# Kernel tuning notes

Measured on AMD Instinct MI355X. Metric: run time of the kernel, lower is better.

## Reference

```python
import jax, jax.numpy as jnp
import numpy as np

NUM_EXPERTS = 8
TOP_K = 2
HIDDEN = 2048
INTER = 7168
NUM_TOKENS = 8192


def setup_inputs() -> dict:
    key = jax.random.key(0)
    k0, k1, k2, k3, k4 = jax.random.split(key, 5)
    hidden_states = jax.random.normal(k0, (NUM_TOKENS, HIDDEN), dtype=jnp.float32)
    gate_w = jax.random.normal(k1, (NUM_EXPERTS, HIDDEN), dtype=jnp.float32) / 10.0
    w1 = jax.random.normal(k2, (NUM_EXPERTS, INTER, HIDDEN), dtype=jnp.float32) / 10.0
    w3 = jax.random.normal(k3, (NUM_EXPERTS, INTER, HIDDEN), dtype=jnp.float32) / 10.0
    w2 = jax.random.normal(k4, (NUM_EXPERTS, HIDDEN, INTER), dtype=jnp.float32) / 10.0
    return {"hidden_states": hidden_states, "gate_w": gate_w, "w1": w1, "w3": w3, "w2": w2}


def reference(hidden_states, gate_w, w1, w3, w2):
    x = hidden_states  # [T, H]
    num_experts = gate_w.shape[0]
    # router
    router_logits = x @ gate_w.T  # [T, E]
    probs = jax.nn.softmax(router_logits.astype(jnp.float32), axis=-1)
    top_w, top_i = jax.lax.top_k(probs, TOP_K)              # [T, K]
    top_w = top_w / jnp.sum(top_w, axis=-1, keepdims=True)  # renormalize
    top_w = top_w.astype(x.dtype)
    # dense [T, E] routing weight (0 for unselected experts)
    expert_ids = jnp.arange(num_experts)
    w_dense = jnp.sum(
        jnp.where(top_i[:, :, None] == expert_ids[None, None, :], top_w[:, :, None], 0.0),
        axis=1,
    )  # [T, E]
    out = jnp.zeros_like(x)
    for e in range(num_experts):
        g = jax.nn.silu(x @ w1[e].T) * (x @ w3[e].T)  # [T, I]
        out = out + w_dense[:, e:e + 1] * (g @ w2[e].T)
    return out
```

## Files before the change

kernel.cpp:

```cpp
#include <hip/hip_runtime.h>

#define NTOK 8192
#define HID 2048
#define ITR 7168
#define NE 8
#define BK32 32
#define TILE32 (128 * BK32)

typedef __attribute__((ext_vector_type(8))) short short8;
typedef __attribute__((ext_vector_type(8))) __bf16 bf16x8;
typedef __attribute__((ext_vector_type(4))) float f32x4;

__device__ __forceinline__ unsigned short f2bf(float f) {
  unsigned int u = __float_as_uint(f);
  u += 0x7FFFu + ((u >> 16) & 1u);
  return (unsigned short)(u >> 16);
}

__device__ __forceinline__ f32x4 mfma_bf16(short8 a, short8 b, f32x4 c) {
  union U { short8 s; bf16x8 b; };
  U ua; ua.s = a;
  U ub; ub.s = b;
  return __builtin_amdgcn_mfma_f32_16x16x32_bf16(ua.b, ub.b, c, 0, 0, 0);
}

typedef __attribute__((address_space(1))) const unsigned int g_u32;
typedef __attribute__((address_space(3))) unsigned int l_u32;

__device__ __forceinline__ void gload16(const unsigned short* src, unsigned short* dst) {
  __builtin_amdgcn_global_load_lds((g_u32*)src, (l_u32*)dst, 16, 0, 0);
}

__device__ __forceinline__ short8 read_frag32(const unsigned short* base, int row, int kelem) {
  int slot = ((row << 2) + (kelem >> 3)) ^ (row & 7);
  return *reinterpret_cast<const short8*>(reinterpret_cast<const char*>(base) + slot * 16);
}

__device__ __forceinline__ void slot_src(int s, int* row, int* c) {
  int r0 = ((s >> 2) ^ (s >> 4)) & 1;
  *row = ((s >> 2) & ~1) | r0;
  *c = ((s ^ r0) & 1) | ((((s >> 1) ^ (s >> 3)) & 1) << 1);
}

#define VMCNT(N) asm volatile("s_waitcnt vmcnt(" #N ")" ::: "memory")
#define BARRIER()                         \
  do {                                    \
    __builtin_amdgcn_s_barrier();         \
    asm volatile("" ::: "memory");        \
  } while (0)

__global__ __launch_bounds__(256) void moe_router(
    const float* __restrict__ x, const float* __restrict__ gw,
    int* __restrict__ cnt, int* __restrict__ pair_token, float* __restrict__ pair_w) {
  int wave = threadIdx.x >> 6;
  int lane = threadIdx.x & 63;
  int t = blockIdx.x * 4 + wave;
  const float4* xr = reinterpret_cast<const float4*>(x + (size_t)t * HID);
  float acc[NE];
#pragma unroll
  for (int e = 0; e < NE; ++e) acc[e] = 0.f;
#pragma unroll
  for (int j = 0; j < 8; ++j) {
    int c = lane + 64 * j;
    float4 xv = xr[c];
#pragma unroll
    for (int e = 0; e < NE; ++e) {
      float4 gv = reinterpret_cast<const float4*>(gw + (size_t)e * HID)[c];
      acc[e] += xv.x * gv.x + xv.y * gv.y + xv.z * gv.z + xv.w * gv.w;
    }
  }
#pragma unroll
  for (int e = 0; e < NE; ++e) {
    float s = acc[e];
#pragma unroll
    for (int m = 32; m > 0; m >>= 1) s += __shfl_xor(s, m);
    acc[e] = s;
  }
  if (lane == 0) {
    int e0 = 0; float l0 = acc[0];
#pragma unroll
    for (int e = 1; e < NE; ++e) if (acc[e] > l0) { l0 = acc[e]; e0 = e; }
    int e1 = -1; float l1 = -3.0e38f;
#pragma unroll
    for (int e = 0; e < NE; ++e) if (e != e0 && acc[e] > l1) { l1 = acc[e]; e1 = e; }
    float z = __expf(l1 - l0);
    float w0 = 1.f / (1.f + z);
    float w1 = z / (1.f + z);
    int p0 = atomicAdd(&cnt[e0], 1);
    pair_token[e0 * NTOK + p0] = t;
    pair_w[e0 * NTOK + p0] = w0;
    int p1 = atomicAdd(&cnt[e1], 1);
    pair_token[e1 * NTOK + p1] = t;
    pair_w[e1 * NTOK + p1] = w1;
  }
}

__global__ void moe_scan(const int* __restrict__ cnt, int* __restrict__ base) {
  if (threadIdx.x == 0) {
    int s = 0;
#pragma unroll
    for (int e = 0; e < NE; ++e) { base[e] = s; s += cnt[e]; }
  }
}

__global__ __launch_bounds__(256) void moe_cvt(const float* __restrict__ src,
                                               unsigned short* __restrict__ dst) {
  size_t i = (size_t)blockIdx.x * 256 + threadIdx.x;
  const float4* p = reinterpret_cast<const float4*>(src) + i * 2;
  float4 a = p[0], b = p[1];
  union { unsigned short us[8]; short8 v; } u;
  u.us[0] = f2bf(a.x); u.us[1] = f2bf(a.y); u.us[2] = f2bf(a.z); u.us[3] = f2bf(a.w);
  u.us[4] = f2bf(b.x); u.us[5] = f2bf(b.y); u.us[6] = f2bf(b.z); u.us[7] = f2bf(b.w);
  reinterpret_cast<short8*>(dst)[i] = u.v;
}


__global__ __launch_bounds__(256, 2) void moe_gemm1_e(
    const unsigned short* __restrict__ xb, const unsigned short* __restrict__ w1b,
    const unsigned short* __restrict__ w3b, const int* __restrict__ cnt,
    const int* __restrict__ base, const int* __restrict__ pair_token,
    unsigned short* __restrict__ g) {
  int e = blockIdx.z;
  int n_e = cnt[e];
  int rowTile = blockIdx.x;
  if (rowTile * 128 >= n_e) return;
  int colTile = blockIdx.y;

  __shared__ unsigned short lds[3 * 3 * TILE32];

  int tid = threadIdx.x;
  int lane = tid & 63;
  int wv = tid >> 6;
  int wr = wv >> 1, wc = wv & 1;
  int lr = lane & 15;
  int lk = (lane >> 4) * 8;

  int slotP = e * NTOK + rowTile * 128;
  int slotG = base[e] + rowTile * 128;
  const unsigned short* w1e = w1b + (size_t)e * ITR * HID + (size_t)colTile * 128 * HID;
  const unsigned short* w3e = w3b + (size_t)e * ITR * HID + (size_t)colTile * 128 * HID;

  const unsigned short* a_s[2];
  const unsigned short* b1_s[2];
  const unsigned short* b3_s[2];
#pragma unroll
  for (int i = 0; i < 2; ++i) {
    int s = wv * 128 + i * 64 + lane;
    int row, c;
    slot_src(s, &row, &c);
    int tok = pair_token[slotP + ((rowTile * 128 + row < n_e) ? row : 0)];
    a_s[i] = xb + (size_t)tok * HID + c * 8;
    b1_s[i] = w1e + (size_t)row * HID + c * 8;
    b3_s[i] = w3e + (size_t)row * HID + c * 8;
  }

  f32x4 acc1[4][4], acc3[4][4];
#pragma unroll
  for (int m = 0; m < 4; ++m)
#pragma unroll
    for (int n = 0; n < 4; ++n) {
      acc1[m][n] = (f32x4){0.f, 0.f, 0.f, 0.f};
      acc3[m][n] = (f32x4){0.f, 0.f, 0.f, 0.f};
    }

#define STAGE1(buf, koff)                                                        \
  do {                                                                           \
    unsigned short* Lb = lds + (buf) * 3 * TILE32 + wv * 1024;                   \
    _Pragma("unroll") for (int i = 0; i < 2; ++i) {                              \
      gload16(a_s[i] + (koff), Lb + i * 512);                                    \
      gload16(b1_s[i] + (koff), Lb + TILE32 + i * 512);                          \
      gload16(b3_s[i] + (koff), Lb + 2 * TILE32 + i * 512);                      \
    }                                                                            \
  } while (0)

  const int nt = HID / BK32;
  STAGE1(0, 0);
  STAGE1(1, BK32);

  for (int t = 0; t < nt; ++t) {
    if (t + 1 < nt) VMCNT(6); else VMCNT(0);
    BARRIER();

    const unsigned short* A = lds + (t % 3) * 3 * TILE32;
    const unsigned short* B1 = A + TILE32;
    const unsigned short* B3 = A + 2 * TILE32;
    short8 av[4];
#pragma unroll
    for (int m = 0; m < 4; ++m) av[m] = read_frag32(A, wr * 64 + m * 16 + lr, lk);
#pragma unroll
    for (int n = 0; n < 4; ++n) {
      short8 b1v = read_frag32(B1, wc * 64 + n * 16 + lr, lk);
      short8 b3v = read_frag32(B3, wc * 64 + n * 16 + lr, lk);
#pragma unroll
      for (int m = 0; m < 4; ++m) {
        acc1[m][n] = mfma_bf16(av[m], b1v, acc1[m][n]);
        acc3[m][n] = mfma_bf16(av[m], b3v, acc3[m][n]);
      }
    }

    if (t + 2 < nt) STAGE1((t + 2) % 3, (t + 2) * BK32);
  }
#undef STAGE1

#pragma unroll
  for (int m = 0; m < 4; ++m) {
    int rbase = wr * 64 + m * 16 + ((lane >> 4) << 2);
#pragma unroll
    for (int r = 0; r < 4; ++r) {
      int rt = rbase + r;
      if (rowTile * 128 + rt < n_e) {
        unsigned short* grow = g + (size_t)(slotG + rt) * ITR + colTile * 128 + wc * 64;
#pragma unroll
        for (int n = 0; n < 4; ++n) {
          float h1 = acc1[m][n][r], h3 = acc3[m][n][r];
          float sl = h1 / (1.f + __expf(-h1));
          grow[n * 16 + lr] = f2bf(sl * h3);
        }
      }
    }
  }
}

__global__ __launch_bounds__(256, 3) void moe_gemm2_e(
    const unsigned short* __restrict__ g, const unsigned short* __restrict__ w2b,
    const int* __restrict__ cnt, const int* __restrict__ base,
    const int* __restrict__ pair_token, const float* __restrict__ pair_w,
    float* __restrict__ out) {
  int e = blockIdx.z;
  int n_e = cnt[e];
  int rowTile = blockIdx.x;
  if (rowTile * 128 >= n_e) return;
  int colTile = blockIdx.y;

  __shared__ unsigned short lds[3 * 2 * TILE32];

  int tid = threadIdx.x;
  int lane = tid & 63;
  int wv = tid >> 6;
  int wr = wv >> 1, wc = wv & 1;
  int lr = lane & 15;
  int lk = (lane >> 4) * 8;

  int slotP = e * NTOK + rowTile * 128;
  int slotG = base[e] + rowTile * 128;
  const unsigned short* w2e = w2b + (size_t)e * HID * ITR + (size_t)colTile * 128 * ITR;

  const unsigned short* a_s[2];
  const unsigned short* b_s[2];
#pragma unroll
  for (int i = 0; i < 2; ++i) {
    int s = wv * 128 + i * 64 + lane;
    int row, c;
    slot_src(s, &row, &c);
    int rclamp = (rowTile * 128 + row < n_e) ? row : 0;
    a_s[i] = g + (size_t)(slotG + rclamp) * ITR + c * 8;
    b_s[i] = w2e + (size_t)row * ITR + c * 8;
  }

  f32x4 acc[4][4];
#pragma unroll
  for (int m = 0; m < 4; ++m)
#pragma unroll
    for (int n = 0; n < 4; ++n) acc[m][n] = (f32x4){0.f, 0.f, 0.f, 0.f};

#define STAGE2(buf, koff)                                                        \
  do {                                                                           \
    unsigned short* Lb = lds + (buf) * 2 * TILE32 + wv * 1024;                   \
    _Pragma("unroll") for (int i = 0; i < 2; ++i) {                              \
      gload16(a_s[i] + (koff), Lb + i * 512);                                    \
      gload16(b_s[i] + (koff), Lb + TILE32 + i * 512);                           \
    }                                                                            \
  } while (0)

  const int nt = ITR / BK32;
  STAGE2(0, 0);
  STAGE2(1, BK32);

  for (int t = 0; t < nt; ++t) {
    if (t + 1 < nt) VMCNT(4); else VMCNT(0);
    BARRIER();

    const unsigned short* A = lds + (t % 3) * 2 * TILE32;
    const unsigned short* B = A + TILE32;
    short8 av[4];
#pragma unroll
    for (int m = 0; m < 4; ++m) av[m] = read_frag32(A, wr * 64 + m * 16 + lr, lk);
#pragma unroll
    for (int n = 0; n < 4; ++n) {
      short8 bv = read_frag32(B, wc * 64 + n * 16 + lr, lk);
#pragma unroll
      for (int m = 0; m < 4; ++m) acc[m][n] = mfma_bf16(av[m], bv, acc[m][n]);
    }

    if (t + 2 < nt) STAGE2((t + 2) % 3, (t + 2) * BK32);
  }
#undef STAGE2

#pragma unroll
  for (int m = 0; m < 4; ++m) {
    int rbase = wr * 64 + m * 16 + ((lane >> 4) << 2);
#pragma unroll
    for (int r = 0; r < 4; ++r) {
      int rt = rbase + r;
      if (rowTile * 128 + rt < n_e) {
        int slot = slotP + rt;
        int tok = pair_token[slot];
        float wgt = pair_w[slot];
        float* orow = out + (size_t)tok * HID + colTile * 128 + wc * 64;
#pragma unroll
        for (int n = 0; n < 4; ++n) atomicAdd(&orow[n * 16 + lr], wgt * acc[m][n][r]);
      }
    }
  }
}


extern "C" void kernel_launch(void* const* d_in, const int* in_sizes, int n_in,
                              void* d_out, int out_size, void* d_ws, size_t ws_size,
                              hipStream_t stream) {
  const float* x = (const float*)d_in[0];
  const float* gate_w = (const float*)d_in[1];
  const float* w1 = (const float*)d_in[2];
  const float* w3 = (const float*)d_in[3];
  const float* w2 = (const float*)d_in[4];
  float* out = (float*)d_out;

  char* ws = (char*)d_ws;
  const size_t WEL = (size_t)NE * ITR * HID;
  const size_t G_BYTES = (size_t)NTOK * 2 * ITR * 2;
  const size_t XB_BYTES = (size_t)NTOK * HID * 2;
  const size_t PAIR_BYTES = (size_t)NE * NTOK * 4;
  const size_t WB_BYTES = WEL * 2;

  unsigned short* g = (unsigned short*)ws;
  unsigned short* xb = (unsigned short*)(ws + G_BYTES);
  int* pair_token = (int*)(ws + G_BYTES + XB_BYTES);
  float* pair_w = (float*)(ws + G_BYTES + XB_BYTES + PAIR_BYTES);
  int* cnt = (int*)(ws + G_BYTES + XB_BYTES + 2 * PAIR_BYTES);
  int* base = cnt + NE;
  char* wbase = ws + G_BYTES + XB_BYTES + 2 * PAIR_BYTES + 256;
  unsigned short* w1b = (unsigned short*)wbase;
  unsigned short* w3b = (unsigned short*)(wbase + WB_BYTES);
  unsigned short* w2b = (unsigned short*)(wbase + 2 * WB_BYTES);

  hipMemsetAsync(cnt, 0, 2 * NE * sizeof(int), stream);
  hipMemsetAsync(d_out, 0, (size_t)NTOK * HID * sizeof(float), stream);

  moe_router<<<NTOK / 4, 256, 0, stream>>>(x, gate_w, cnt, pair_token, pair_w);
  moe_scan<<<1, 64, 0, stream>>>(cnt, base);
  moe_cvt<<<(NTOK * HID) / 2048, 256, 0, stream>>>(x, xb);

  const int WGRID = (int)(WEL / 2048);
  moe_cvt<<<WGRID, 256, 0, stream>>>(w1, w1b);
  moe_cvt<<<WGRID, 256, 0, stream>>>(w3, w3b);
  moe_cvt<<<WGRID, 256, 0, stream>>>(w2, w2b);

  moe_gemm1_e<<<dim3(NTOK / 128, ITR / 128, NE), 256, 0, stream>>>(
      xb, w1b, w3b, cnt, base, pair_token, g);
  moe_gemm2_e<<<dim3(NTOK / 128, HID / 128, NE), 256, 0, stream>>>(
      g, w2b, cnt, base, pair_token, pair_w, out);
}
```

Measured before the change: 3.379 ms.

## Enlarge MoE GEMM tiles, deepen pipeline, replace scatter atomics with combine kernel

```diff
diff --git a/kernel.cpp b/kernel.cpp
--- a/kernel.cpp
+++ b/kernel.cpp
@@ -5,7 +5,6 @@
 #define ITR 7168
 #define NE 8
 #define BK32 32
-#define TILE32 (128 * BK32)
 
 typedef __attribute__((ext_vector_type(8))) short short8;
 typedef __attribute__((ext_vector_type(8))) __bf16 bf16x8;
@@ -51,7 +50,8 @@
 
 __global__ __launch_bounds__(256) void moe_router(
     const float* __restrict__ x, const float* __restrict__ gw,
-    int* __restrict__ cnt, int* __restrict__ pair_token, float* __restrict__ pair_w) {
+    int* __restrict__ cnt, int* __restrict__ pair_token, float* __restrict__ pair_w,
+    int4* __restrict__ tok_ep) {
   int wave = threadIdx.x >> 6;
   int lane = threadIdx.x & 63;
   int t = blockIdx.x * 4 + wave;
@@ -92,6 +92,7 @@
     int p1 = atomicAdd(&cnt[e1], 1);
     pair_token[e1 * NTOK + p1] = t;
     pair_w[e1 * NTOK + p1] = w1;
+    tok_ep[t] = make_int4(e0, e1, p0, p1);
   }
 }
 
@@ -115,7 +116,9 @@
 }
 
 
-__global__ __launch_bounds__(256, 2) void moe_gemm1_e(
+#define G1_BUF 16384
+
+__global__ __launch_bounds__(512, 2) void moe_gemm1_f(
     const unsigned short* __restrict__ xb, const unsigned short* __restrict__ w1b,
     const unsigned short* __restrict__ w3b, const int* __restrict__ cnt,
     const int* __restrict__ base, const int* __restrict__ pair_token,
@@ -123,35 +126,41 @@
   int e = blockIdx.z;
   int n_e = cnt[e];
   int rowTile = blockIdx.x;
-  if (rowTile * 128 >= n_e) return;
+  if (rowTile * 256 >= n_e) return;
   int colTile = blockIdx.y;
 
-  __shared__ unsigned short lds[3 * 3 * TILE32];
+  __shared__ unsigned short lds[4 * G1_BUF];
 
   int tid = threadIdx.x;
   int lane = tid & 63;
   int wv = tid >> 6;
-  int wr = wv >> 1, wc = wv & 1;
+  int wr = wv >> 1;
+  int wc = wv & 1;
   int lr = lane & 15;
   int lk = (lane >> 4) * 8;
 
-  int slotP = e * NTOK + rowTile * 128;
-  int slotG = base[e] + rowTile * 128;
+  int slotP = e * NTOK + rowTile * 256;
+  int slotG = base[e] + rowTile * 256;
   const unsigned short* w1e = w1b + (size_t)e * ITR * HID + (size_t)colTile * 128 * HID;
   const unsigned short* w3e = w3b + (size_t)e * ITR * HID + (size_t)colTile * 128 * HID;
 
   const unsigned short* a_s[2];
-  const unsigned short* b1_s[2];
-  const unsigned short* b3_s[2];
+  const unsigned short* b1_s;
+  const unsigned short* b3_s;
 #pragma unroll
   for (int i = 0; i < 2; ++i) {
-    int s = wv * 128 + i * 64 + lane;
+    int s = i * 512 + wv * 64 + lane;
     int row, c;
     slot_src(s, &row, &c);
-    int tok = pair_token[slotP + ((rowTile * 128 + row < n_e) ? row : 0)];
+    int tok = pair_token[slotP + ((rowTile * 256 + row < n_e) ? row : 0)];
     a_s[i] = xb + (size_t)tok * HID + c * 8;
-    b1_s[i] = w1e + (size_t)row * HID + c * 8;
-    b3_s[i] = w3e + (size_t)row * HID + c * 8;
+  }
+  {
+    int s = wv * 64 + lane;
+    int row, c;
+    slot_src(s, &row, &c);
+    b1_s = w1e + (size_t)row * HID + c * 8;
+    b3_s = w3e + (size_t)row * HID + c * 8;
   }
 
   f32x4 acc1[4][4], acc3[4][4];
@@ -163,27 +172,29 @@
       acc3[m][n] = (f32x4){0.f, 0.f, 0.f, 0.f};
     }
 
-#define STAGE1(buf, koff)                                                        \
-  do {                                                                           \
-    unsigned short* Lb = lds + (buf) * 3 * TILE32 + wv * 1024;                   \
-    _Pragma("unroll") for (int i = 0; i < 2; ++i) {                              \
-      gload16(a_s[i] + (koff), Lb + i * 512);                                    \
-      gload16(b1_s[i] + (koff), Lb + TILE32 + i * 512);                          \
-      gload16(b3_s[i] + (koff), Lb + 2 * TILE32 + i * 512);                      \
-    }                                                                            \
+#define STAGE1(buf, koff)                                                  \
+  do {                                                                     \
+    unsigned short* Lb = lds + (buf) * G1_BUF;                             \
+    gload16(a_s[0] + (koff), Lb + (wv * 64) * 8);                          \
+    gload16(a_s[1] + (koff), Lb + (512 + wv * 64) * 8);                    \
+    gload16(b1_s + (koff), Lb + 8192 + (wv * 64) * 8);                     \
+    gload16(b3_s + (koff), Lb + 12288 + (wv * 64) * 8);                    \
   } while (0)
 
   const int nt = HID / BK32;
   STAGE1(0, 0);
   STAGE1(1, BK32);
+  STAGE1(2, 2 * BK32);
 
   for (int t = 0; t < nt; ++t) {
-    if (t + 1 < nt) VMCNT(6); else VMCNT(0);
+    if (t + 2 < nt) VMCNT(8);
+    else if (t + 1 < nt) VMCNT(4);
+    else VMCNT(0);
     BARRIER();
 
-    const unsigned short* A = lds + (t % 3) * 3 * TILE32;
-    const unsigned short* B1 = A + TILE32;
-    const unsigned short* B3 = A + 2 * TILE32;
+    const unsigned short* A = lds + (t & 3) * G1_BUF;
+    const unsigned short* B1 = A + 8192;
+    const unsigned short* B3 = A + 12288;
     short8 av[4];
 #pragma unroll
     for (int m = 0; m < 4; ++m) av[m] = read_frag32(A, wr * 64 + m * 16 + lr, lk);
@@ -198,7 +209,7 @@
       }
     }
 
-    if (t + 2 < nt) STAGE1((t + 2) % 3, (t + 2) * BK32);
+    if (t + 3 < nt) STAGE1((t + 3) & 3, (t + 3) * BK32);
   }
 #undef STAGE1
 
@@ -208,7 +219,7 @@
 #pragma unroll
     for (int r = 0; r < 4; ++r) {
       int rt = rbase + r;
-      if (rowTile * 128 + rt < n_e) {
+      if (rowTile * 256 + rt < n_e) {
         unsigned short* grow = g + (size_t)(slotG + rt) * ITR + colTile * 128 + wc * 64;
 #pragma unroll
         for (int n = 0; n < 4; ++n) {
@@ -221,96 +232,117 @@
   }
 }
 
-__global__ __launch_bounds__(256, 3) void moe_gemm2_e(
+#define G2_BUF 16384
+
+__global__ __launch_bounds__(512, 2) void moe_gemm2_f(
     const unsigned short* __restrict__ g, const unsigned short* __restrict__ w2b,
     const int* __restrict__ cnt, const int* __restrict__ base,
-    const int* __restrict__ pair_token, const float* __restrict__ pair_w,
-    float* __restrict__ out) {
+    const float* __restrict__ pair_w, float* __restrict__ part) {
   int e = blockIdx.z;
   int n_e = cnt[e];
   int rowTile = blockIdx.x;
-  if (rowTile * 128 >= n_e) return;
+  if (rowTile * 256 >= n_e) return;
   int colTile = blockIdx.y;
 
-  __shared__ unsigned short lds[3 * 2 * TILE32];
+  __shared__ unsigned short lds[4 * G2_BUF];
 
   int tid = threadIdx.x;
   int lane = tid & 63;
   int wv = tid >> 6;
-  int wr = wv >> 1, wc = wv & 1;
+  int wr = wv >> 2;
+  int wc = wv & 3;
   int lr = lane & 15;
   int lk = (lane >> 4) * 8;
 
-  int slotP = e * NTOK + rowTile * 128;
-  int slotG = base[e] + rowTile * 128;
-  const unsigned short* w2e = w2b + (size_t)e * HID * ITR + (size_t)colTile * 128 * ITR;
+  int slotP = e * NTOK + rowTile * 256;
+  int slotG = base[e] + rowTile * 256;
+  const unsigned short* w2e = w2b + (size_t)e * HID * ITR + (size_t)colTile * 256 * ITR;
 
   const unsigned short* a_s[2];
   const unsigned short* b_s[2];
 #pragma unroll
   for (int i = 0; i < 2; ++i) {
-    int s = wv * 128 + i * 64 + lane;
+    int s = i * 512 + wv * 64 + lane;
     int row, c;
     slot_src(s, &row, &c);
-    int rclamp = (rowTile * 128 + row < n_e) ? row : 0;
+    int rclamp = (rowTile * 256 + row < n_e) ? row : 0;
     a_s[i] = g + (size_t)(slotG + rclamp) * ITR + c * 8;
     b_s[i] = w2e + (size_t)row * ITR + c * 8;
   }
 
-  f32x4 acc[4][4];
-#pragma unroll
-  for (int m = 0; m < 4; ++m)
+  f32x4 acc[8][4];
+#pragma unroll
+  for (int m = 0; m < 8; ++m)
 #pragma unroll
     for (int n = 0; n < 4; ++n) acc[m][n] = (f32x4){0.f, 0.f, 0.f, 0.f};
 
-#define STAGE2(buf, koff)                                                        \
-  do {                                                                           \
-    unsigned short* Lb = lds + (buf) * 2 * TILE32 + wv * 1024;                   \
-    _Pragma("unroll") for (int i = 0; i < 2; ++i) {                              \
-      gload16(a_s[i] + (koff), Lb + i * 512);                                    \
-      gload16(b_s[i] + (koff), Lb + TILE32 + i * 512);                           \
-    }                                                                            \
+#define STAGE2(buf, koff)                                                  \
+  do {                                                                     \
+    unsigned short* Lb = lds + (buf) * G2_BUF;                             \
+    gload16(a_s[0] + (koff), Lb + (wv * 64) * 8);                          \
+    gload16(a_s[1] + (koff), Lb + (512 + wv * 64) * 8);                    \
+    gload16(b_s[0] + (koff), Lb + 8192 + (wv * 64) * 8);                   \
+    gload16(b_s[1] + (koff), Lb + 8192 + (512 + wv * 64) * 8);             \
   } while (0)
 
   const int nt = ITR / BK32;
   STAGE2(0, 0);
   STAGE2(1, BK32);
+  STAGE2(2, 2 * BK32);
 
   for (int t = 0; t < nt; ++t) {
-    if (t + 1 < nt) VMCNT(4); else VMCNT(0);
+    if (t + 2 < nt) VMCNT(8);
+    else if (t + 1 < nt) VMCNT(4);
+    else VMCNT(0);
     BARRIER();
 
-    const unsigned short* A = lds + (t % 3) * 2 * TILE32;
-    const unsigned short* B = A + TILE32;
-    short8 av[4];
-#pragma unroll
-    for (int m = 0; m < 4; ++m) av[m] = read_frag32(A, wr * 64 + m * 16 + lr, lk);
+    const unsigned short* A = lds + (t & 3) * G2_BUF;
+    const unsigned short* B = A + 8192;
+    short8 av[8];
+#pragma unroll
+    for (int m = 0; m < 8; ++m) av[m] = read_frag32(A, wr * 128 + m * 16 + lr, lk);
 #pragma unroll
     for (int n = 0; n < 4; ++n) {
       short8 bv = read_frag32(B, wc * 64 + n * 16 + lr, lk);
 #pragma unroll
-      for (int m = 0; m < 4; ++m) acc[m][n] = mfma_bf16(av[m], bv, acc[m][n]);
-    }
-
-    if (t + 2 < nt) STAGE2((t + 2) % 3, (t + 2) * BK32);
+      for (int m = 0; m < 8; ++m) acc[m][n] = mfma_bf16(av[m], bv, acc[m][n]);
+    }
+
+    if (t + 3 < nt) STAGE2((t + 3) & 3, (t + 3) * BK32);
   }
 #undef STAGE2
 
 #pragma unroll
-  for (int m = 0; m < 4; ++m) {
-    int rbase = wr * 64 + m * 16 + ((lane >> 4) << 2);
+  for (int m = 0; m < 8; ++m) {
+    int rbase = wr * 128 + m * 16 + ((lane >> 4) << 2);
 #pragma unroll
     for (int r = 0; r < 4; ++r) {
       int rt = rbase + r;
-      if (rowTile * 128 + rt < n_e) {
-        int slot = slotP + rt;
-        int tok = pair_token[slot];
-        float wgt = pair_w[slot];
-        float* orow = out + (size_t)tok * HID + colTile * 128 + wc * 64;
-#pragma unroll
-        for (int n = 0; n < 4; ++n) atomicAdd(&orow[n * 16 + lr], wgt * acc[m][n][r]);
+      if (rowTile * 256 + rt < n_e) {
+        float wgt = pair_w[slotP + rt];
+        float* prow = part + (size_t)(slotG + rt) * HID + colTile * 256 + wc * 64;
+#pragma unroll
+        for (int n = 0; n < 4; ++n) prow[n * 16 + lr] = wgt * acc[m][n][r];
       }
     }
+  }
+}
+
+__global__ __launch_bounds__(256) void moe_combine(
+    const float* __restrict__ part, const int4* __restrict__ tok_ep,
+    const int* __restrict__ base, float* __restrict__ out) {
+  int t = blockIdx.x;
+  int4 ep = tok_ep[t];
+  int s0 = base[ep.x] + ep.z;
+  int s1 = base[ep.y] + ep.w;
+  const float4* p0 = reinterpret_cast<const float4*>(part + (size_t)s0 * HID);
+  const float4* p1 = reinterpret_cast<const float4*>(part + (size_t)s1 * HID);
+  float4* o = reinterpret_cast<float4*>(out + (size_t)t * HID);
+#pragma unroll
+  for (int i = 0; i < 2; ++i) {
+    int idx = threadIdx.x + i * 256;
+    float4 a = p0[idx], b = p1[idx];
+    o[idx] = make_float4(a.x + b.x, a.y + b.y, a.z + b.z, a.w + b.w);
   }
 }
 
@@ -330,23 +362,25 @@
   const size_t G_BYTES = (size_t)NTOK * 2 * ITR * 2;
   const size_t XB_BYTES = (size_t)NTOK * HID * 2;
   const size_t PAIR_BYTES = (size_t)NE * NTOK * 4;
+  const size_t TOKEP_BYTES = (size_t)NTOK * 16;
   const size_t WB_BYTES = WEL * 2;
 
   unsigned short* g = (unsigned short*)ws;
   unsigned short* xb = (unsigned short*)(ws + G_BYTES);
   int* pair_token = (int*)(ws + G_BYTES + XB_BYTES);
   float* pair_w = (float*)(ws + G_BYTES + XB_BYTES + PAIR_BYTES);
-  int* cnt = (int*)(ws + G_BYTES + XB_BYTES + 2 * PAIR_BYTES);
+  int4* tok_ep = (int4*)(ws + G_BYTES + XB_BYTES + 2 * PAIR_BYTES);
+  int* cnt = (int*)(ws + G_BYTES + XB_BYTES + 2 * PAIR_BYTES + TOKEP_BYTES);
   int* base = cnt + NE;
-  char* wbase = ws + G_BYTES + XB_BYTES + 2 * PAIR_BYTES + 256;
+  char* wbase = ws + G_BYTES + XB_BYTES + 2 * PAIR_BYTES + TOKEP_BYTES + 256;
   unsigned short* w1b = (unsigned short*)wbase;
   unsigned short* w3b = (unsigned short*)(wbase + WB_BYTES);
   unsigned short* w2b = (unsigned short*)(wbase + 2 * WB_BYTES);
+  float* part = (float*)wbase;
 
   hipMemsetAsync(cnt, 0, 2 * NE * sizeof(int), stream);
-  hipMemsetAsync(d_out, 0, (size_t)NTOK * HID * sizeof(float), stream);
-
-  moe_router<<<NTOK / 4, 256, 0, stream>>>(x, gate_w, cnt, pair_token, pair_w);
+
+  moe_router<<<NTOK / 4, 256, 0, stream>>>(x, gate_w, cnt, pair_token, pair_w, tok_ep);
   moe_scan<<<1, 64, 0, stream>>>(cnt, base);
   moe_cvt<<<(NTOK * HID) / 2048, 256, 0, stream>>>(x, xb);
 
@@ -355,8 +389,9 @@
   moe_cvt<<<WGRID, 256, 0, stream>>>(w3, w3b);
   moe_cvt<<<WGRID, 256, 0, stream>>>(w2, w2b);
 
-  moe_gemm1_e<<<dim3(NTOK / 128, ITR / 128, NE), 256, 0, stream>>>(
+  moe_gemm1_f<<<dim3(NTOK / 256, ITR / 128, NE), 512, 0, stream>>>(
       xb, w1b, w3b, cnt, base, pair_token, g);
-  moe_gemm2_e<<<dim3(NTOK / 128, HID / 128, NE), 256, 0, stream>>>(
-      g, w2b, cnt, base, pair_token, pair_w, out);
-}
+  moe_gemm2_f<<<dim3(NTOK / 256, HID / 256, NE), 512, 0, stream>>>(
+      g, w2b, cnt, base, pair_w, part);
+  moe_combine<<<NTOK, 256, 0, stream>>>(part, tok_ep, base, out);
+}
```

After: 5.402 ms. 1.6x slower.
